# Kernel optimization log

Measured on AMD Instinct MI355X. Metric: run time of the kernel, lower is better.

The kernel has to match this reference:

```python
import jax, jax.numpy as jnp
import numpy as np

B, S, D = 4096, 200, 64
EPS = 1e-3  # keras BatchNormalization default epsilon

def setup_inputs() -> dict:
    key = jax.random.key(0)
    ks = jax.random.split(key, 8)
    return {
        "em": jax.random.normal(ks[0], (B, D), jnp.float32),
        "eu": jax.random.normal(ks[1], (B, D), jnp.float32),
        "Xu": jax.random.normal(ks[2], (B, S, D), jnp.float32),
        "W1": jax.random.normal(ks[3], (4 * D, 64), jnp.float32) * 0.05,
        "b1": jnp.zeros((64,), jnp.float32),
        "W2": jax.random.normal(ks[4], (64, 32), jnp.float32) * 0.1,
        "b2": jnp.zeros((32,), jnp.float32),
        "W3": jax.random.normal(ks[5], (32, 1), jnp.float32) * 0.1,
        "b3": jnp.zeros((1,), jnp.float32),
        "gamma": jnp.ones((2 * D,), jnp.float32),
        "beta": jnp.zeros((2 * D,), jnp.float32),
        "mov_mean": jnp.zeros((2 * D,), jnp.float32),
        "mov_var": jnp.ones((2 * D,), jnp.float32),
    }

def reference(em, eu, Xu, W1, b1, W2, b2, W3, b3, gamma, beta, mov_mean, mov_var):
    # DIN attention: query = em tiled over seq, key = value = Xu
    q = jnp.broadcast_to(em[:, None, :], Xu.shape)            # [B,S,D]
    info = jnp.concatenate([q, Xu, q - Xu, q * Xu], axis=-1)  # [B,S,4D]
    h = jax.nn.relu(info @ W1 + b1)                           # [B,S,64]
    h = jax.nn.relu(h @ W2 + b2)                              # [B,S,32]
    logits = (h @ W3 + b3)[..., 0]                            # [B,S]
    w = jax.nn.softmax(logits, axis=-1)                       # [B,S]
    pooled = jnp.einsum('bs,bsd->bd', w, Xu)                  # [B,D]
    info_all = jnp.concatenate([pooled, em], axis=-1)         # [B,2D]
    bn = (info_all - mov_mean) * jax.lax.rsqrt(mov_var + EPS) * gamma + beta
    return jnp.concatenate([bn, eu], axis=-1)                 # [B,2D+Du]
```

## Files before the change

### kernel.cpp

```cpp
#include <hip/hip_runtime.h>
#include <hip/hip_bf16.h>
#include <math.h>

typedef __bf16 bf16_t;
typedef bf16_t bf16x4 __attribute__((ext_vector_type(4)));
typedef bf16_t bf16x8 __attribute__((ext_vector_type(8)));
typedef float  f32x4  __attribute__((ext_vector_type(4)));

#define SEQ 200
#define SP  208
#define DD  64
#define RS  72

#define MFMA(a, b, c) __builtin_amdgcn_mfma_f32_16x16x32_bf16((a), (b), (c), 0, 0, 0)

__global__ __launch_bounds__(256) void din_kernel(
    const float* __restrict__ em, const float* __restrict__ eu,
    const float* __restrict__ Xu, const float* __restrict__ W1,
    const float* __restrict__ b1, const float* __restrict__ W2,
    const float* __restrict__ b2, const float* __restrict__ W3,
    const float* __restrict__ b3, const float* __restrict__ gam,
    const float* __restrict__ bet, const float* __restrict__ mmean,
    const float* __restrict__ mvar, float* __restrict__ out)
{
  __shared__ __align__(16) bf16_t A1[SP * RS];
  __shared__ __align__(16) bf16_t A2[SP * RS];
  __shared__ float em_s[DD];
  __shared__ float qWp[4][DD];
  __shared__ float qW[DD];
  __shared__ float logits[SP];
  __shared__ float red[8];
  __shared__ float wpool[4][DD];

  const int tid  = threadIdx.x;
  const int b    = blockIdx.x;
  const int lane = tid & 63;
  const int wid  = tid >> 6;
  const int g    = lane >> 4;
  const int l16  = lane & 15;

  if (tid < DD) em_s[tid] = em[(size_t)b * DD + tid];
  for (int i = tid; i < 8 * DD; i += 256) {
    int r = SEQ + (i >> 6), c = i & 63;
    A1[r * RS + c] = (bf16_t)0.f;
    A2[r * RS + c] = (bf16_t)0.f;
  }

  const int n1 = 16 * wid + l16;
  bf16x8 bX[2], bQ[2];
  #pragma unroll
  for (int c = 0; c < 2; ++c)
    #pragma unroll
    for (int j = 0; j < 8; ++j) {
      int k = 32 * c + 8 * g + j;
      bX[c][j] = (bf16_t)(W1[(64 + k) * 64 + n1] - W1[(128 + k) * 64 + n1]);
      bQ[c][j] = (bf16_t)(W1[(192 + k) * 64 + n1]);
    }
  bf16x8 bW2f[2][2];
  #pragma unroll
  for (int c = 0; c < 2; ++c)
    #pragma unroll
    for (int u = 0; u < 2; ++u)
      #pragma unroll
      for (int j = 0; j < 8; ++j) {
        int k = 32 * c + 8 * g + j;
        bW2f[c][u][j] = (bf16_t)(W2[k * 32 + 16 * u + l16]);
      }
  const float b2v0 = b2[l16], b2v1 = b2[16 + l16];
  const float w3v0 = W3[l16], w3v1 = W3[16 + l16];
  const float b3s  = b3[0];

  __syncthreads();

  const float4* Xr = (const float4*)(Xu + (size_t)b * SEQ * DD);
  for (int v = tid; v < SEQ * DD / 4; v += 256) {
    int s  = v >> 4;
    int c4 = (v & 15) * 4;
    float4 x = Xr[v];
    bf16x4 xa, xq;
    xa[0] = (bf16_t)x.x; xa[1] = (bf16_t)x.y;
    xa[2] = (bf16_t)x.z; xa[3] = (bf16_t)x.w;
    xq[0] = (bf16_t)(x.x * em_s[c4 + 0]); xq[1] = (bf16_t)(x.y * em_s[c4 + 1]);
    xq[2] = (bf16_t)(x.z * em_s[c4 + 2]); xq[3] = (bf16_t)(x.w * em_s[c4 + 3]);
    *(bf16x4*)&A1[s * RS + c4] = xa;
    *(bf16x4*)&A2[s * RS + c4] = xq;
  }
  {
    int j = tid & 63, p = tid >> 6;
    float acc = 0.f;
    for (int d = 16 * p; d < 16 * p + 16; ++d)
      acc += em_s[d] * (W1[d * 64 + j] + W1[(128 + d) * 64 + j]);
    qWp[p][j] = acc;
  }
  __syncthreads();
  if (tid < DD)
    qW[tid] = qWp[0][tid] + qWp[1][tid] + qWp[2][tid] + qWp[3][tid] + b1[tid];
  __syncthreads();

  f32x4 acc[13];
  #pragma unroll
  for (int t = 0; t < 13; ++t) {
    f32x4 a = {0.f, 0.f, 0.f, 0.f};
    int rb = (16 * t + l16) * RS + 8 * g;
    bf16x8 a10 = *(const bf16x8*)&A1[rb];
    bf16x8 a11 = *(const bf16x8*)&A1[rb + 32];
    bf16x8 a20 = *(const bf16x8*)&A2[rb];
    bf16x8 a21 = *(const bf16x8*)&A2[rb + 32];
    a = MFMA(a10, bX[0], a);
    a = MFMA(a11, bX[1], a);
    a = MFMA(a20, bQ[0], a);
    a = MFMA(a21, bQ[1], a);
    acc[t] = a;
  }
  __syncthreads();

  {
    float qn = qW[n1];
    #pragma unroll
    for (int t = 0; t < 13; ++t)
      #pragma unroll
      for (int r = 0; r < 4; ++r) {
        float v = acc[t][r] + qn;
        v = v > 0.f ? v : 0.f;
        A2[(16 * t + 4 * g + r) * RS + n1] = (bf16_t)v;
      }
  }
  __syncthreads();

  for (int t = wid; t < 13; t += 4) {
    int rb = (16 * t + l16) * RS + 8 * g;
    bf16x8 h0 = *(const bf16x8*)&A2[rb];
    bf16x8 h1 = *(const bf16x8*)&A2[rb + 32];
    f32x4 a0 = {0.f, 0.f, 0.f, 0.f}, a1 = {0.f, 0.f, 0.f, 0.f};
    a0 = MFMA(h0, bW2f[0][0], a0);
    a0 = MFMA(h1, bW2f[1][0], a0);
    a1 = MFMA(h0, bW2f[0][1], a1);
    a1 = MFMA(h1, bW2f[1][1], a1);
    #pragma unroll
    for (int r = 0; r < 4; ++r) {
      float p0 = fmaxf(a0[r] + b2v0, 0.f) * w3v0;
      float p1 = fmaxf(a1[r] + b2v1, 0.f) * w3v1;
      float pr = p0 + p1;
      pr += __shfl_xor(pr, 1);
      pr += __shfl_xor(pr, 2);
      pr += __shfl_xor(pr, 4);
      pr += __shfl_xor(pr, 8);
      if (l16 == 0) logits[16 * t + 4 * g + r] = pr + b3s;
    }
  }
  __syncthreads();

  float lv = (tid < SEQ) ? logits[tid] : -INFINITY;
  float mx = lv;
  #pragma unroll
  for (int o = 32; o > 0; o >>= 1) mx = fmaxf(mx, __shfl_xor(mx, o));
  if (lane == 0) red[wid] = mx;
  __syncthreads();
  mx = fmaxf(fmaxf(red[0], red[1]), fmaxf(red[2], red[3]));
  float e = (tid < SEQ) ? __expf(lv - mx) : 0.f;
  float ssum = e;
  #pragma unroll
  for (int o = 32; o > 0; o >>= 1) ssum += __shfl_xor(ssum, o);
  if (lane == 0) red[4 + wid] = ssum;
  __syncthreads();
  float inv = 1.f / (red[4] + red[5] + red[6] + red[7]);
  if (tid < SEQ) logits[tid] = e * inv;
  __syncthreads();

  {
    int d = tid & 63, p = wid;
    float ps = 0.f;
    for (int s = p; s < SEQ; s += 4)
      ps += logits[s] * (float)A1[s * RS + d];
    wpool[p][d] = ps;
  }
  __syncthreads();

  if (tid < 192) {
    float v;
    if (tid < 128) {
      float x = (tid < 64)
          ? (wpool[0][tid] + wpool[1][tid] + wpool[2][tid] + wpool[3][tid])
          : em_s[tid - 64];
      v = (x - mmean[tid]) * rsqrtf(mvar[tid] + 1e-3f) * gam[tid] + bet[tid];
    } else {
      v = eu[(size_t)b * 64 + (tid - 128)];
    }
    out[(size_t)b * 192 + tid] = v;
  }
}

extern "C" void kernel_launch(void* const* d_in, const int* in_sizes, int n_in,
                              void* d_out, int out_size, void* d_ws, size_t ws_size,
                              hipStream_t stream) {
  const float* em = (const float*)d_in[0];
  const float* eu = (const float*)d_in[1];
  const float* Xu = (const float*)d_in[2];
  const float* W1 = (const float*)d_in[3];
  const float* b1 = (const float*)d_in[4];
  const float* W2 = (const float*)d_in[5];
  const float* b2 = (const float*)d_in[6];
  const float* W3 = (const float*)d_in[7];
  const float* b3 = (const float*)d_in[8];
  const float* ga = (const float*)d_in[9];
  const float* be = (const float*)d_in[10];
  const float* mm = (const float*)d_in[11];
  const float* mv = (const float*)d_in[12];
  int B = in_sizes[0] / DD;
  din_kernel<<<B, 256, 0, stream>>>(em, eu, Xu, W1, b1, W2, b2, W3, b3,
                                    ga, be, mm, mv, (float*)d_out);
}
```

Measured before the change: 402.0 us.

## Fold query scaling into per-batch W1 weights, precompute weights in prep kernel

Uses (Xu*em)@W1d = Xu@(diag(em)W1d) to fold the query-dependent terms into the first-layer weight matrix. The X tile then needs only one bf16 LDS buffer and two MFMAs per tile instead of four. A separate prep kernel pre-transposes and converts W1 and W2 to bf16 and computes the per-batch query bias Q, so the main kernel no longer does strided scalar weight loads or the em@W reduction. Xu is also kept in registers for the pooling step, and LDS use is halved so more blocks can be resident (launch_bounds 256,4). The cost is an extra kernel launch, workspace traffic, and a barrier inside the first-layer loop, since layer-1 results now overwrite the same buffer.

```diff
diff --git a/kernel.cpp b/kernel.cpp
--- a/kernel.cpp
+++ b/kernel.cpp
@@ -14,23 +14,47 @@
 
 #define MFMA(a, b, c) __builtin_amdgcn_mfma_f32_16x16x32_bf16((a), (b), (c), 0, 0, 0)
 
-__global__ __launch_bounds__(256) void din_kernel(
+__global__ __launch_bounds__(256) void prep_kernel(
+    const float* __restrict__ em, const float* __restrict__ W1,
+    const float* __restrict__ b1, const float* __restrict__ W2,
+    bf16_t* __restrict__ Wbc, bf16_t* __restrict__ W1dt,
+    bf16_t* __restrict__ W2t, float* __restrict__ Q)
+{
+  const int tid = threadIdx.x;
+  if (blockIdx.x == 0) {
+    for (int i = tid; i < 64 * 64; i += 256) {
+      int n = i >> 6, k = i & 63;
+      Wbc[i]  = (bf16_t)(W1[(64 + k) * 64 + n] - W1[(128 + k) * 64 + n]);
+      W1dt[i] = (bf16_t)(W1[(192 + k) * 64 + n]);
+    }
+    for (int i = tid; i < 32 * 64; i += 256) {
+      int n = i >> 6, k = i & 63;
+      W2t[i] = (bf16_t)(W2[k * 32 + n]);
+    }
+  } else {
+    int b = (blockIdx.x - 1) * 4 + (tid >> 6);
+    int n = tid & 63;
+    float acc = b1[n];
+    for (int d = 0; d < 64; ++d)
+      acc += em[(size_t)b * 64 + d] * (W1[d * 64 + n] + W1[(128 + d) * 64 + n]);
+    Q[(size_t)b * 64 + n] = acc;
+  }
+}
+
+__global__ __launch_bounds__(256, 4) void din_kernel(
     const float* __restrict__ em, const float* __restrict__ eu,
-    const float* __restrict__ Xu, const float* __restrict__ W1,
-    const float* __restrict__ b1, const float* __restrict__ W2,
-    const float* __restrict__ b2, const float* __restrict__ W3,
-    const float* __restrict__ b3, const float* __restrict__ gam,
-    const float* __restrict__ bet, const float* __restrict__ mmean,
-    const float* __restrict__ mvar, float* __restrict__ out)
+    const float* __restrict__ Xu, const float* __restrict__ b2,
+    const float* __restrict__ W3, const float* __restrict__ b3,
+    const float* __restrict__ gam, const float* __restrict__ bet,
+    const float* __restrict__ mmean, const float* __restrict__ mvar,
+    const bf16_t* __restrict__ Wbc, const bf16_t* __restrict__ W1dt,
+    const bf16_t* __restrict__ W2t, const float* __restrict__ Q,
+    float* __restrict__ out)
 {
-  __shared__ __align__(16) bf16_t A1[SP * RS];
-  __shared__ __align__(16) bf16_t A2[SP * RS];
-  __shared__ float em_s[DD];
-  __shared__ float qWp[4][DD];
-  __shared__ float qW[DD];
+  __shared__ __align__(16) bf16_t A[SP * RS];
   __shared__ float logits[SP];
   __shared__ float red[8];
-  __shared__ float wpool[4][DD];
+  float* part = (float*)A;
 
   const int tid  = threadIdx.x;
   const int b    = blockIdx.x;
@@ -38,99 +62,86 @@
   const int wid  = tid >> 6;
   const int g    = lane >> 4;
   const int l16  = lane & 15;
-
-  if (tid < DD) em_s[tid] = em[(size_t)b * DD + tid];
+  const int n1   = 16 * wid + l16;
+
   for (int i = tid; i < 8 * DD; i += 256) {
     int r = SEQ + (i >> 6), c = i & 63;
-    A1[r * RS + c] = (bf16_t)0.f;
-    A2[r * RS + c] = (bf16_t)0.f;
-  }
-
-  const int n1 = 16 * wid + l16;
-  bf16x8 bX[2], bQ[2];
+    A[r * RS + c] = (bf16_t)0.f;
+  }
+
+  const bf16x8* Wbc8  = (const bf16x8*)Wbc;
+  const bf16x8* W1dt8 = (const bf16x8*)W1dt;
+  const bf16x8* W2t8  = (const bf16x8*)W2t;
+  bf16x8 bB[2];
+  #pragma unroll
+  for (int c = 0; c < 2; ++c) {
+    bf16x8 wbc = Wbc8[n1 * 8 + 4 * c + g];
+    bf16x8 w1d = W1dt8[n1 * 8 + 4 * c + g];
+    float4 e0 = *(const float4*)&em[(size_t)b * DD + 32 * c + 8 * g];
+    float4 e1 = *(const float4*)&em[(size_t)b * DD + 32 * c + 8 * g + 4];
+    bB[c][0] = (bf16_t)((float)wbc[0] + e0.x * (float)w1d[0]);
+    bB[c][1] = (bf16_t)((float)wbc[1] + e0.y * (float)w1d[1]);
+    bB[c][2] = (bf16_t)((float)wbc[2] + e0.z * (float)w1d[2]);
+    bB[c][3] = (bf16_t)((float)wbc[3] + e0.w * (float)w1d[3]);
+    bB[c][4] = (bf16_t)((float)wbc[4] + e1.x * (float)w1d[4]);
+    bB[c][5] = (bf16_t)((float)wbc[5] + e1.y * (float)w1d[5]);
+    bB[c][6] = (bf16_t)((float)wbc[6] + e1.z * (float)w1d[6]);
+    bB[c][7] = (bf16_t)((float)wbc[7] + e1.w * (float)w1d[7]);
+  }
+  bf16x8 bW2f[2][2];
   #pragma unroll
   for (int c = 0; c < 2; ++c)
     #pragma unroll
-    for (int j = 0; j < 8; ++j) {
-      int k = 32 * c + 8 * g + j;
-      bX[c][j] = (bf16_t)(W1[(64 + k) * 64 + n1] - W1[(128 + k) * 64 + n1]);
-      bQ[c][j] = (bf16_t)(W1[(192 + k) * 64 + n1]);
-    }
-  bf16x8 bW2f[2][2];
-  #pragma unroll
-  for (int c = 0; c < 2; ++c)
-    #pragma unroll
     for (int u = 0; u < 2; ++u)
-      #pragma unroll
-      for (int j = 0; j < 8; ++j) {
-        int k = 32 * c + 8 * g + j;
-        bW2f[c][u][j] = (bf16_t)(W2[k * 32 + 16 * u + l16]);
-      }
+      bW2f[c][u] = W2t8[(16 * u + l16) * 8 + 4 * c + g];
+
+  const float qn   = Q[(size_t)b * DD + n1];
   const float b2v0 = b2[l16], b2v1 = b2[16 + l16];
   const float w3v0 = W3[l16], w3v1 = W3[16 + l16];
   const float b3s  = b3[0];
 
-  __syncthreads();
-
   const float4* Xr = (const float4*)(Xu + (size_t)b * SEQ * DD);
-  for (int v = tid; v < SEQ * DD / 4; v += 256) {
-    int s  = v >> 4;
-    int c4 = (v & 15) * 4;
-    float4 x = Xr[v];
-    bf16x4 xa, xq;
-    xa[0] = (bf16_t)x.x; xa[1] = (bf16_t)x.y;
-    xa[2] = (bf16_t)x.z; xa[3] = (bf16_t)x.w;
-    xq[0] = (bf16_t)(x.x * em_s[c4 + 0]); xq[1] = (bf16_t)(x.y * em_s[c4 + 1]);
-    xq[2] = (bf16_t)(x.z * em_s[c4 + 2]); xq[3] = (bf16_t)(x.w * em_s[c4 + 3]);
-    *(bf16x4*)&A1[s * RS + c4] = xa;
-    *(bf16x4*)&A2[s * RS + c4] = xq;
-  }
-  {
-    int j = tid & 63, p = tid >> 6;
-    float acc = 0.f;
-    for (int d = 16 * p; d < 16 * p + 16; ++d)
-      acc += em_s[d] * (W1[d * 64 + j] + W1[(128 + d) * 64 + j]);
-    qWp[p][j] = acc;
-  }
-  __syncthreads();
-  if (tid < DD)
-    qW[tid] = qWp[0][tid] + qWp[1][tid] + qWp[2][tid] + qWp[3][tid] + b1[tid];
-  __syncthreads();
-
-  f32x4 acc[13];
-  #pragma unroll
+  bf16x4 xr[13];
+  #pragma unroll
+  for (int k = 0; k < 13; ++k) {
+    int v = tid + 256 * k;
+    if (v < SEQ * DD / 4) {
+      int s  = v >> 4;
+      int c4 = (v & 15) * 4;
+      float4 x = Xr[v];
+      bf16x4 xa;
+      xa[0] = (bf16_t)x.x; xa[1] = (bf16_t)x.y;
+      xa[2] = (bf16_t)x.z; xa[3] = (bf16_t)x.w;
+      xr[k] = xa;
+      *(bf16x4*)&A[s * RS + c4] = xa;
+    } else {
+      xr[k][0] = (bf16_t)0.f; xr[k][1] = (bf16_t)0.f;
+      xr[k][2] = (bf16_t)0.f; xr[k][3] = (bf16_t)0.f;
+    }
+  }
+  __syncthreads();
+
   for (int t = 0; t < 13; ++t) {
+    int rb = (16 * t + l16) * RS + 8 * g;
+    bf16x8 a0 = *(const bf16x8*)&A[rb];
+    bf16x8 a1 = *(const bf16x8*)&A[rb + 32];
     f32x4 a = {0.f, 0.f, 0.f, 0.f};
-    int rb = (16 * t + l16) * RS + 8 * g;
-    bf16x8 a10 = *(const bf16x8*)&A1[rb];
-    bf16x8 a11 = *(const bf16x8*)&A1[rb + 32];
-    bf16x8 a20 = *(const bf16x8*)&A2[rb];
-    bf16x8 a21 = *(const bf16x8*)&A2[rb + 32];
-    a = MFMA(a10, bX[0], a);
-    a = MFMA(a11, bX[1], a);
-    a = MFMA(a20, bQ[0], a);
-    a = MFMA(a21, bQ[1], a);
-    acc[t] = a;
-  }
-  __syncthreads();
-
-  {
-    float qn = qW[n1];
-    #pragma unroll
-    for (int t = 0; t < 13; ++t)
-      #pragma unroll
-      for (int r = 0; r < 4; ++r) {
-        float v = acc[t][r] + qn;
-        v = v > 0.f ? v : 0.f;
-        A2[(16 * t + 4 * g + r) * RS + n1] = (bf16_t)v;
-      }
+    a = MFMA(a0, bB[0], a);
+    a = MFMA(a1, bB[1], a);
+    __syncthreads();
+    #pragma unroll
+    for (int r = 0; r < 4; ++r) {
+      float v = a[r] + qn;
+      v = v > 0.f ? v : 0.f;
+      A[(16 * t + 4 * g + r) * RS + n1] = (bf16_t)v;
+    }
   }
   __syncthreads();
 
   for (int t = wid; t < 13; t += 4) {
     int rb = (16 * t + l16) * RS + 8 * g;
-    bf16x8 h0 = *(const bf16x8*)&A2[rb];
-    bf16x8 h1 = *(const bf16x8*)&A2[rb + 32];
+    bf16x8 h0 = *(const bf16x8*)&A[rb];
+    bf16x8 h1 = *(const bf16x8*)&A[rb + 32];
     f32x4 a0 = {0.f, 0.f, 0.f, 0.f}, a1 = {0.f, 0.f, 0.f, 0.f};
     a0 = MFMA(h0, bW2f[0][0], a0);
     a0 = MFMA(h1, bW2f[1][0], a0);
@@ -168,23 +179,36 @@
   __syncthreads();
 
   {
-    int d = tid & 63, p = wid;
-    float ps = 0.f;
-    for (int s = p; s < SEQ; s += 4)
-      ps += logits[s] * (float)A1[s * RS + d];
-    wpool[p][d] = ps;
+    float4 ps = {0.f, 0.f, 0.f, 0.f};
+    #pragma unroll
+    for (int k = 0; k < 13; ++k) {
+      int v = tid + 256 * k;
+      if (v < SEQ * DD / 4) {
+        float w = logits[(tid >> 4) + 16 * k];
+        ps.x += w * (float)xr[k][0];
+        ps.y += w * (float)xr[k][1];
+        ps.z += w * (float)xr[k][2];
+        ps.w += w * (float)xr[k][3];
+      }
+    }
+    *(float4*)&part[(tid >> 4) * 68 + (tid & 15) * 4] = ps;
   }
   __syncthreads();
 
   if (tid < 192) {
     float v;
     if (tid < 128) {
-      float x = (tid < 64)
-          ? (wpool[0][tid] + wpool[1][tid] + wpool[2][tid] + wpool[3][tid])
-          : em_s[tid - 64];
+      float x;
+      if (tid < 64) {
+        x = 0.f;
+        #pragma unroll
+        for (int r = 0; r < 16; ++r) x += part[r * 68 + tid];
+      } else {
+        x = em[(size_t)b * DD + (tid - 64)];
+      }
       v = (x - mmean[tid]) * rsqrtf(mvar[tid] + 1e-3f) * gam[tid] + bet[tid];
     } else {
-      v = eu[(size_t)b * 64 + (tid - 128)];
+      v = eu[(size_t)b * DD + (tid - 128)];
     }
     out[(size_t)b * 192 + tid] = v;
   }
@@ -207,6 +231,13 @@
   const float* mm = (const float*)d_in[11];
   const float* mv = (const float*)d_in[12];
   int B = in_sizes[0] / DD;
-  din_kernel<<<B, 256, 0, stream>>>(em, eu, Xu, W1, b1, W2, b2, W3, b3,
-                                    ga, be, mm, mv, (float*)d_out);
+
+  float*  Q    = (float*)d_ws;
+  bf16_t* Wbc  = (bf16_t*)((char*)d_ws + (size_t)B * 64 * 4);
+  bf16_t* W1dt = Wbc  + 64 * 64;
+  bf16_t* W2t  = W1dt + 64 * 64;
+
+  prep_kernel<<<1 + B / 4, 256, 0, stream>>>(em, W1, b1, W2, Wbc, W1dt, W2t, Q);
+  din_kernel<<<B, 256, 0, stream>>>(em, eu, Xu, b2, W3, b3, ga, be, mm, mv,
+                                    Wbc, W1dt, W2t, Q, (float*)d_out);
 }
```

Result: faster. 332.6 us (-17.3%).
